# Performance work log

Measured on AMD Instinct MI355X. Metric: run time of the kernel, lower is better.

The kernel has to match this reference:

```python
import jax, jax.numpy as jnp
import numpy as np

NUM_HEADS = 16


def setup_inputs() -> dict:
    key = jax.random.key(0)
    ks = jax.random.split(key, 6)
    dim = 1024
    B, N = 4, 4096
    s = 1.0 / np.sqrt(dim)
    return {
        "x": jax.random.normal(ks[0], (B, N, dim), dtype=jnp.float32),
        "Wq": jax.random.normal(ks[1], (dim, dim), dtype=jnp.float32) * s,
        "Wk": jax.random.normal(ks[2], (dim, dim), dtype=jnp.float32) * s,
        "Wv": jax.random.normal(ks[3], (dim, dim), dtype=jnp.float32) * s,
        "Wo": jax.random.normal(ks[4], (dim, dim), dtype=jnp.float32) * s,
        "bo": jnp.zeros((dim,), dtype=jnp.float32),
    }


def reference(x, Wq, Wk, Wv, Wo, bo):
    # STAtten (linear attention) branch, no SNN, dropout = 0 (identity in eval).
    B, N, C = x.shape
    H = NUM_HEADS
    D = C // H
    scale = D ** (-0.5)

    def heads(W):
        # torch nn.Linear: y = x @ W.T ; then [B,N,H,D] -> [B,H,N,D]
        y = jnp.einsum('bnc,oc->bno', x, W)
        return y.reshape(B, N, H, D).transpose(0, 2, 1, 3)

    q = heads(Wq)
    k = heads(Wk)
    v = heads(Wv)

    kv = jnp.einsum('bhnd,bhne->bhde', k, v) * scale  # [B,H,D,D]
    out = jnp.einsum('bhnd,bhde->bhne', q, kv)        # [B,H,N,D]

    out = out.transpose(0, 2, 1, 3).reshape(B, N, C)
    return jnp.einsum('bnc,oc->bno', out, Wo) + bo
```

## Files before the change

kernel.cpp:

```cpp
#include <hip/hip_runtime.h>
#include <hip/hip_bf16.h>
#include <math.h>

typedef __hip_bfloat16 bf16;
typedef float f32x4 __attribute__((ext_vector_type(4)));
typedef short s16x8 __attribute__((ext_vector_type(8)));

typedef const __attribute__((address_space(1))) void* as1cvp;
typedef __attribute__((address_space(3))) void* as3vp;

__device__ __forceinline__ unsigned short f2bf(float f) {
  unsigned u = __float_as_uint(f);
  u += 0x7FFFu + ((u >> 16) & 1u);
  return (unsigned short)(u >> 16);
}
__device__ __forceinline__ float bf2f(unsigned short s) {
  return __uint_as_float(((unsigned)s) << 16);
}

__device__ __forceinline__ void gpu_barrier() {
  asm volatile("" ::: "memory");
  __builtin_amdgcn_s_barrier();
  asm volatile("" ::: "memory");
}

__device__ __forceinline__ void tri_decode(int xt, int* ti_out, int* tj_out) {
  int tj = (int)((sqrtf(8.0f * (float)xt + 1.0f) - 1.0f) * 0.5f);
  int tri = tj * (tj + 1) / 2;
  if (xt < tri) { --tj; tri = tj * (tj + 1) / 2; }
  else if (xt >= tri + tj + 1) { ++tj; tri = tj * (tj + 1) / 2; }
  *ti_out = xt - tri;
  *tj_out = tj;
}

__global__ __launch_bounds__(256) void cast_transpose(const float* __restrict__ x,
                                                      unsigned short* __restrict__ xb,
                                                      unsigned short* __restrict__ xT) {
  __shared__ unsigned short tl[128 * 136];
  const int n0 = blockIdx.x * 128, d0 = blockIdx.y * 128, b = blockIdx.z;
  const int t = threadIdx.x;

  const int rr0 = t >> 4;
  const int u   = t & 15;
  const int dd  = u * 8;
#pragma unroll
  for (int it = 0; it < 8; ++it) {
    const int rr = rr0 + it * 16;
    const float* src = x + ((long)(b * 4096 + n0 + rr)) * 1024 + d0 + dd;
    f32x4 v0 = *(const f32x4*)src;
    f32x4 v1 = *(const f32x4*)(src + 4);
    s16x8 o;
    o[0] = (short)f2bf(v0[0]); o[1] = (short)f2bf(v0[1]);
    o[2] = (short)f2bf(v0[2]); o[3] = (short)f2bf(v0[3]);
    o[4] = (short)f2bf(v1[0]); o[5] = (short)f2bf(v1[1]);
    o[6] = (short)f2bf(v1[2]); o[7] = (short)f2bf(v1[3]);
    *(s16x8*)&xb[((long)(b * 4096 + n0 + rr)) * 1024 + d0 + dd] = o;
    const int phys = u ^ (rr >> 3);
    *(s16x8*)&tl[rr * 136 + phys * 8] = o;
  }
  __syncthreads();

  const int nblk = t & 15, dblk = t >> 4;
  s16x8 row[8];
#pragma unroll
  for (int j = 0; j < 8; ++j) {
    const int n = nblk * 8 + j;
    const int phys = dblk ^ nblk;
    row[j] = *(const s16x8*)&tl[n * 136 + phys * 8];
  }
#pragma unroll
  for (int c = 0; c < 8; ++c) {
    s16x8 col;
#pragma unroll
    for (int j = 0; j < 8; ++j) col[j] = row[j][c];
    *(s16x8*)&xT[((long)(b * 1024 + d0 + dblk * 8 + c)) * 4096 + n0 + nblk * 8] = col;
  }
}

__global__ __launch_bounds__(256) void cast_weights(const float* __restrict__ Wq,
                                                    const float* __restrict__ Wk,
                                                    const float* __restrict__ Wv,
                                                    const float* __restrict__ Wo,
                                                    unsigned short* __restrict__ Wkb,
                                                    unsigned short* __restrict__ Wvb,
                                                    unsigned short* __restrict__ Wqb,
                                                    unsigned short* __restrict__ Wob) {
  const int i = blockIdx.x * 256 + threadIdx.x;
  const int seg = blockIdx.y;
  const long flat = (long)i * 8;
  const float* src = (seg == 0) ? Wk : (seg == 1) ? Wv : (seg == 2) ? Wq : Wo;
  f32x4 v0 = *(const f32x4*)&src[flat];
  f32x4 v1 = *(const f32x4*)&src[flat + 4];
  s16x8 o;
  o[0] = (short)f2bf(v0[0]); o[1] = (short)f2bf(v0[1]);
  o[2] = (short)f2bf(v0[2]); o[3] = (short)f2bf(v0[3]);
  o[4] = (short)f2bf(v1[0]); o[5] = (short)f2bf(v1[1]);
  o[6] = (short)f2bf(v1[2]); o[7] = (short)f2bf(v1[3]);
  unsigned short* dst = (seg == 0) ? Wkb : (seg == 1) ? Wvb : (seg == 2) ? Wqb : Wob;
  *(s16x8*)&dst[flat] = o;
}

template<bool OUTF32>
__global__ __launch_bounds__(512, 2) void gemm256(
    const bf16* __restrict__ A, int lda, long aOffY, long aOffZ,
    const bf16* __restrict__ Bt, int ldb, long btOffY, long btOffZ,
    void* __restrict__ Cv, int ldc, long cOffY, long cOffZ,
    const float* __restrict__ bias, int K, int NtN, int gridmode)
{
  __shared__ char lds[131072];

  const int Nx = gridDim.x, Ny = gridDim.y;
  const int lin = blockIdx.x + Nx * (blockIdx.y + Ny * blockIdx.z);
  const int tot = Nx * Ny * gridDim.z;
  const int swz = (lin & 7) * (tot >> 3) + (lin >> 3);
  const int xt = swz % Nx;
  const int r2 = swz / Nx;
  const int y = r2 % Ny, z = r2 / Ny;
  int ti, tj;
  if (gridmode == 1) {
    ti = (int)((0x3221110000ULL >> (4 * xt)) & 15);
    tj = (int)((0x3323213210ULL >> (4 * xt)) & 15);
  } else { ti = xt / NtN; tj = xt % NtN; }
  const int bm = ti * 256, bn = tj * 256;

  A  += (long)z * aOffZ + (long)y * aOffY;
  Bt += (long)z * btOffZ + (long)y * btOffY;

  const int tid  = threadIdx.x;
  const int wid  = tid >> 6;
  const int lane = tid & 63;
  const int wm = wid >> 2;
  const int wn = wid & 3;
  const int frow = lane & 15;
  const int fkb  = (lane >> 4) << 4;
  const unsigned xorv = (unsigned)((lane & 7) << 4);

  const int q0 = (tid * 16) ^ (((tid >> 3) & 7) << 4);
  const int q1 = (8192 + tid * 16) ^ (((tid >> 3) & 7) << 4);
  const int srow0 = q0 >> 7, scol0 = (q0 & 127) >> 1;
  const int srow1 = q1 >> 7, scol1 = (q1 & 127) >> 1;
  const bf16* ag0 = A  + (long)(bm + srow0) * lda + scol0;
  const bf16* ag1 = A  + (long)(bm + srow1) * lda + scol1;
  const bf16* bg0 = Bt + (long)(bn + srow0) * ldb + scol0;
  const bf16* bg1 = Bt + (long)(bn + srow1) * ldb + scol1;

#define STAGE_A(buf, half, kk) do {                                                  \
    __builtin_amdgcn_global_load_lds((as1cvp)(ag0 + (long)(half)*128*lda + (kk)),    \
        (as3vp)(lds + (buf)*32768 + (half)*16384 + wid*1024), 16, 0, 0);             \
    __builtin_amdgcn_global_load_lds((as1cvp)(ag1 + (long)(half)*128*lda + (kk)),    \
        (as3vp)(lds + (buf)*32768 + (half)*16384 + 8192 + wid*1024), 16, 0, 0);      \
  } while (0)
#define STAGE_B(buf, half, kk) do {                                                  \
    __builtin_amdgcn_global_load_lds((as1cvp)(bg0 + (long)(half)*128*ldb + (kk)),    \
        (as3vp)(lds + 65536 + (buf)*32768 + (half)*16384 + wid*1024), 16, 0, 0);     \
    __builtin_amdgcn_global_load_lds((as1cvp)(bg1 + (long)(half)*128*ldb + (kk)),    \
        (as3vp)(lds + 65536 + (buf)*32768 + (half)*16384 + 8192 + wid*1024), 16, 0, 0); \
  } while (0)

  const unsigned paBase = (unsigned)((wm * 64 + frow) * 128 + fkb);
  const unsigned pbBase = (unsigned)(((wn & 1) * 64 + frow) * 128 + fkb);
  const unsigned bHalf  = (unsigned)((wn >> 1) * 16384);

#define RD_A(dst, cur, Mh, mi, kh)                                                   \
  dst = *(const s16x8*)(lds + (cur)*32768 + (Mh)*16384 +                             \
                        ((paBase + (mi)*2048u + (kh)*64u) ^ xorv))
#define RD_B(dst, cur, nj, kh)                                                       \
  dst = *(const s16x8*)(lds + 65536 + (cur)*32768 + bHalf +                          \
                        ((pbBase + (nj)*2048u + (kh)*64u) ^ xorv))

#define MFMA16(base, bb)                                                             \
  __builtin_amdgcn_s_setprio(1);                                                     \
  _Pragma("unroll")                                                                  \
  for (int mi = 0; mi < 4; ++mi)                                                     \
    _Pragma("unroll")                                                                \
    for (int nj = 0; nj < 4; ++nj)                                                   \
      acc[(base) + mi][nj] = __builtin_amdgcn_mfma_f32_16x16x32_bf16(                \
          a[mi], bb[nj], acc[(base) + mi][nj], 0, 0, 0);                             \
  __builtin_amdgcn_s_setprio(0);

#define LGKM0 asm volatile("s_waitcnt lgkmcnt(0)" ::: "memory")
#define VM8   asm volatile("s_waitcnt vmcnt(8)" ::: "memory")

  f32x4 acc[8][4] = {};
  s16x8 a[4], b0[4], b1[4];
  const int NT = K >> 6;

  STAGE_A(0, 0, 0); STAGE_B(0, 0, 0); STAGE_B(0, 1, 0);
  STAGE_A(0, 1, 0);
  {
    const int kk = (NT > 1) ? 64 : 0;
    STAGE_A(1, 0, kk); STAGE_B(1, 0, kk); STAGE_B(1, 1, kk);
  }
  VM8;
  gpu_barrier();

  for (int t = 0; t < NT; ++t) {
    const int cur = t & 1, nxt = cur ^ 1;
    const int k1 = ((t + 1 < NT) ? (t + 1) : 0) * 64;
    const int k2 = ((t + 2 < NT) ? (t + 2) : 0) * 64;

#pragma unroll
    for (int mi = 0; mi < 4; ++mi) RD_A(a[mi], cur, 0, mi, 0);
#pragma unroll
    for (int nj = 0; nj < 4; ++nj) RD_B(b0[nj], cur, nj, 0);
    STAGE_A(nxt, 1, k1);
    gpu_barrier(); LGKM0;
    MFMA16(0, b0)
    gpu_barrier();

#pragma unroll
    for (int mi = 0; mi < 4; ++mi) RD_A(a[mi], cur, 0, mi, 1);
#pragma unroll
    for (int nj = 0; nj < 4; ++nj) RD_B(b1[nj], cur, nj, 1);
    gpu_barrier(); LGKM0;
    MFMA16(0, b1)
    VM8;
    gpu_barrier();

#pragma unroll
    for (int mi = 0; mi < 4; ++mi) RD_A(a[mi], cur, 1, mi, 0);
    STAGE_A(cur, 0, k2); STAGE_B(cur, 0, k2); STAGE_B(cur, 1, k2);
    gpu_barrier(); LGKM0;
    MFMA16(4, b0)
    gpu_barrier();

#pragma unroll
    for (int mi = 0; mi < 4; ++mi) RD_A(a[mi], cur, 1, mi, 1);
    gpu_barrier(); LGKM0;
    MFMA16(4, b1)
    VM8;
    gpu_barrier();
  }

  asm volatile("s_waitcnt vmcnt(0)" ::: "memory");

  const int crow0 = bm + wm * 64 + (lane >> 4) * 4;
  const int ccol0 = bn + wn * 64 + (lane & 15);
  if (OUTF32) {
    float* C = (float*)Cv + (long)z * cOffZ + (long)y * cOffY;
    float bs[4];
#pragma unroll
    for (int j = 0; j < 4; ++j) bs[j] = bias ? bias[ccol0 + j * 16] : 0.0f;
#pragma unroll
    for (int i = 0; i < 8; ++i) {
      const int row = crow0 + (i >> 2) * 128 + (i & 3) * 16;
#pragma unroll
      for (int j = 0; j < 4; ++j) {
        const int col = ccol0 + j * 16;
#pragma unroll
        for (int r = 0; r < 4; ++r)
          C[(long)(row + r) * ldc + col] = acc[i][j][r] + bs[j];
      }
    }
  } else {
    unsigned short* C = (unsigned short*)Cv + (long)z * cOffZ + (long)y * cOffY;
#pragma unroll
    for (int i = 0; i < 8; ++i) {
      const int row = crow0 + (i >> 2) * 128 + (i & 3) * 16;
#pragma unroll
      for (int j = 0; j < 4; ++j) {
        const int col = ccol0 + j * 16;
#pragma unroll
        for (int r = 0; r < 4; ++r)
          C[(long)(row + r) * ldc + col] = f2bf(acc[i][j][r]);
      }
    }
  }
#undef STAGE_A
#undef STAGE_B
#undef RD_A
#undef RD_B
#undef MFMA16
#undef LGKM0
#undef VM8
}

template<int MODE>
__global__ __launch_bounds__(256) void gemm128(
    const bf16* __restrict__ A0, const bf16* __restrict__ B0,
    void* __restrict__ Cv, const float* __restrict__ bias)
{
  __shared__ char lds[65536];

  const int Nx = gridDim.x;
  const int lin = blockIdx.x + Nx * blockIdx.y;
  const int tot = Nx * gridDim.y;
  const int swz = (lin & 7) * (tot >> 3) + (lin >> 3);
  const int xt = swz % Nx, yy = swz / Nx;

  const int lda = (MODE == 0) ? 4096 : 1024;
  const int ldb = lda;
  const int K   = 1024;
  int bm, bn;
  const bf16 *A, *Bt;
  if (MODE == 0) {
    int ti, tj; tri_decode(xt, &ti, &tj);
    bm = ti * 128; bn = tj * 128;
    const int z = yy >> 2, ys = yy & 3;
    A  = A0 + (long)z * 4194304 + ys * 1024;
    Bt = A;
  } else {
    bm = (xt >> 3) * 128; bn = (xt & 7) * 128;
    A  = A0;
    Bt = B0 + (long)yy * 1048576L;
  }

  const int tid  = threadIdx.x;
  const int wid  = tid >> 6;
  const int lane = tid & 63;
  const int wr = (wid >> 1) * 64, wc = (wid & 1) * 64;
  const int frow = lane & 15;
  const int fkb  = (lane >> 4) << 4;
  const unsigned xorv = (unsigned)((lane & 7) << 4);

  const int q0 = (tid * 16) ^ (((tid >> 3) & 7) << 4);
  const int srow0 = q0 >> 7, scol0 = (q0 & 127) >> 1;
  const bf16* ag = A  + (long)(bm + srow0) * lda + scol0;
  const bf16* bg = Bt + (long)(bn + srow0) * ldb + scol0;

#define STG128(buf, kk) do {                                                         \
    _Pragma("unroll")                                                                \
    for (int i = 0; i < 4; ++i) {                                                    \
      __builtin_amdgcn_global_load_lds((as1cvp)(ag + (long)i * 32 * lda + (kk)),     \
          (as3vp)(lds + (buf) * 16384 + i * 4096 + tid * 16), 16, 0, 0);             \
      __builtin_amdgcn_global_load_lds((as1cvp)(bg + (long)i * 32 * ldb + (kk)),     \
          (as3vp)(lds + 32768 + (buf) * 16384 + i * 4096 + tid * 16), 16, 0, 0);     \
    }                                                                                \
  } while (0)

  const unsigned paB = (unsigned)((wr + frow) * 128 + fkb);
  const unsigned pbB = (unsigned)((wc + frow) * 128 + fkb);

  f32x4 acc[4][4] = {};
  const int NT = K >> 6;

  STG128(0, 0);
  asm volatile("s_waitcnt vmcnt(0)" ::: "memory");
  gpu_barrier();

  for (int t = 0; t < NT; ++t) {
    const int cur = t & 1;
    if (t + 1 < NT) STG128(cur ^ 1, (t + 1) * 64);
    s16x8 a[4][2], b[4][2];
#pragma unroll
    for (int mi = 0; mi < 4; ++mi)
#pragma unroll
      for (int kh = 0; kh < 2; ++kh)
        a[mi][kh] = *(const s16x8*)(lds + cur * 16384 +
                                    ((paB + mi * 2048u + kh * 64u) ^ xorv));
#pragma unroll
    for (int nj = 0; nj < 4; ++nj)
#pragma unroll
      for (int kh = 0; kh < 2; ++kh)
        b[nj][kh] = *(const s16x8*)(lds + 32768 + cur * 16384 +
                                    ((pbB + nj * 2048u + kh * 64u) ^ xorv));
    asm volatile("s_waitcnt lgkmcnt(0)" ::: "memory");
#pragma unroll
    for (int mi = 0; mi < 4; ++mi)
#pragma unroll
      for (int nj = 0; nj < 4; ++nj) {
        acc[mi][nj] = __builtin_amdgcn_mfma_f32_16x16x32_bf16(a[mi][0], b[nj][0], acc[mi][nj], 0, 0, 0);
        acc[mi][nj] = __builtin_amdgcn_mfma_f32_16x16x32_bf16(a[mi][1], b[nj][1], acc[mi][nj], 0, 0, 0);
      }
    asm volatile("s_waitcnt vmcnt(0)" ::: "memory");
    gpu_barrier();
  }

  const int r0 = wr + (lane >> 4) * 4;
  const int c0t = wc + (lane & 15);
  if (MODE == 0) {
    unsigned short* C = (unsigned short*)Cv + (long)(yy * 36 + xt) * 16384;
#pragma unroll
    for (int mi = 0; mi < 4; ++mi)
#pragma unroll
      for (int nj = 0; nj < 4; ++nj)
#pragma unroll
        for (int r = 0; r < 4; ++r)
          C[(r0 + mi * 16 + r) * 128 + c0t + nj * 16] = f2bf(acc[mi][nj][r]);
  } else {
    unsigned short* C = (unsigned short*)Cv + (long)yy * 1048576;
#pragma unroll
    for (int mi = 0; mi < 4; ++mi)
#pragma unroll
      for (int nj = 0; nj < 4; ++nj)
#pragma unroll
        for (int r = 0; r < 4; ++r)
          C[(long)(bm + r0 + mi * 16 + r) * 1024 + bn + c0t + nj * 16] =
              f2bf(acc[mi][nj][r]);
  }
#undef STG128
}

__global__ __launch_bounds__(256) void gred128(const unsigned short* __restrict__ Gp,
                                               unsigned short* __restrict__ Gb) {
  const int tile = blockIdx.x >> 2, sub = blockIdx.x & 3;
  const int z = blockIdx.y;
  int ti, tj; tri_decode(tile, &ti, &tj);
  const int t = threadIdx.x;
  const int rr = sub * 32 + (t >> 3);
  const int c0 = (t & 7) * 16;

  float s[16] = {};
#pragma unroll
  for (int y = 0; y < 4; ++y) {
    const unsigned short* p = Gp + ((long)(z * 4 + y) * 36 + tile) * 16384 + rr * 128 + c0;
#pragma unroll
    for (int q = 0; q < 2; ++q) {
      s16x8 v = *(const s16x8*)&p[q * 8];
#pragma unroll
      for (int j = 0; j < 8; ++j) s[q * 8 + j] += bf2f((unsigned short)v[j]);
    }
  }
  unsigned short hi[16];
#pragma unroll
  for (int j = 0; j < 16; ++j) hi[j] = f2bf(s[j]);
  unsigned short* base = Gb + (long)z * 1048576;
  const int R0 = ti * 128 + rr, C0 = tj * 128 + c0;
#pragma unroll
  for (int q = 0; q < 2; ++q)
    *(s16x8*)&base[(long)R0 * 1024 + C0 + q * 8] = *(const s16x8*)&hi[q * 8];
  if (ti != tj) {
#pragma unroll
    for (int j = 0; j < 16; ++j)
      base[(long)(C0 + j) * 1024 + R0] = hi[j];
  }
}

template<int OUTMODE>
__global__ __launch_bounds__(256) void gemm64(
    const bf16* __restrict__ A, int lda, long aOffZ,
    const bf16* __restrict__ Bt, int ldb, long btOffZ,
    void* __restrict__ Cv, int ldc, long cOffZ, int loOff,
    int K, int NtN, int diag, int ksplit)
{
  __shared__ char lds[32768];

  const int Nx = gridDim.x;
  const int lin = blockIdx.x + Nx * blockIdx.y;
  const int tot = Nx * gridDim.y;
  const int swz = (lin & 7) * (tot >> 3) + (lin >> 3);
  const int xt = swz % Nx, y = swz / Nx;
  const int zb = y / ksplit, zs = y % ksplit;
  const int ti = diag ? xt : xt / NtN;
  const int tj = diag ? xt : xt % NtN;
  const int bm = ti * 64, bn = tj * 64;

  A  += (long)zb * aOffZ + (long)zs * K;
  Bt += (long)zb * btOffZ + (long)zs * K;

  const int tid  = threadIdx.x;
  const int wid  = tid >> 6;
  const int lane = tid & 63;
  const int wr = (wid >> 1) * 32, wc = (wid & 1) * 32;
  const int frow = lane & 15;
  const int fkb  = (lane >> 4) << 4;
  const unsigned xorv = (unsigned)((lane & 7) << 4);

  const int q0 = (tid * 16) ^ (((tid >> 3) & 7) << 4);
  const int q1 = (4096 + tid * 16) ^ (((tid >> 3) & 7) << 4);
  const int srow0 = q0 >> 7, scol0 = (q0 & 127) >> 1;
  const int srow1 = q1 >> 7, scol1 = (q1 & 127) >> 1;
  const bf16* ag0 = A  + (long)(bm + srow0) * lda + scol0;
  const bf16* ag1 = A  + (long)(bm + srow1) * lda + scol1;
  const bf16* bg0 = Bt + (long)(bn + srow0) * ldb + scol0;
  const bf16* bg1 = Bt + (long)(bn + srow1) * ldb + scol1;

#define STAGE64(buf, kk) do {                                                        \
    __builtin_amdgcn_global_load_lds((as1cvp)(ag0 + (kk)),                           \
        (as3vp)(lds + (buf)*8192 + wid*1024), 16, 0, 0);                             \
    __builtin_amdgcn_global_load_lds((as1cvp)(ag1 + (kk)),                           \
        (as3vp)(lds + (buf)*8192 + 4096 + wid*1024), 16, 0, 0);                      \
    __builtin_amdgcn_global_load_lds((as1cvp)(bg0 + (kk)),                           \
        (as3vp)(lds + 16384 + (buf)*8192 + wid*1024), 16, 0, 0);                     \
    __builtin_amdgcn_global_load_lds((as1cvp)(bg1 + (kk)),                           \
        (as3vp)(lds + 16384 + (buf)*8192 + 4096 + wid*1024), 16, 0, 0);              \
  } while (0)

  const unsigned paB = (unsigned)((wr + frow) * 128 + fkb);
  const unsigned pbB = (unsigned)((wc + frow) * 128 + fkb);

  f32x4 acc[2][2] = {};
  const int NT = K >> 6;

  STAGE64(0, 0);
  asm volatile("s_waitcnt vmcnt(0)" ::: "memory");
  gpu_barrier();

  for (int t = 0; t < NT; ++t) {
    const int cur = t & 1;
    if (t + 1 < NT) STAGE64(cur ^ 1, (t + 1) * 64);
    s16x8 a[2][2], b[2][2];
#pragma unroll
    for (int mi = 0; mi < 2; ++mi)
#pragma unroll
      for (int kh = 0; kh < 2; ++kh)
        a[mi][kh] = *(const s16x8*)(lds + cur * 8192 +
                                    ((paB + mi * 2048u + kh * 64u) ^ xorv));
#pragma unroll
    for (int nj = 0; nj < 2; ++nj)
#pragma unroll
      for (int kh = 0; kh < 2; ++kh)
        b[nj][kh] = *(const s16x8*)(lds + 16384 + cur * 8192 +
                                    ((pbB + nj * 2048u + kh * 64u) ^ xorv));
    asm volatile("s_waitcnt lgkmcnt(0)" ::: "memory");
#pragma unroll
    for (int mi = 0; mi < 2; ++mi)
#pragma unroll
      for (int nj = 0; nj < 2; ++nj) {
        acc[mi][nj] = __builtin_amdgcn_mfma_f32_16x16x32_bf16(a[mi][0], b[nj][0], acc[mi][nj], 0, 0, 0);
        acc[mi][nj] = __builtin_amdgcn_mfma_f32_16x16x32_bf16(a[mi][1], b[nj][1], acc[mi][nj], 0, 0, 0);
      }
    asm volatile("s_waitcnt vmcnt(0)" ::: "memory");
    gpu_barrier();
  }

  const int r0 = wr + (lane >> 4) * 4;
  const int c0 = wc + (lane & 15);
  if (OUTMODE == 1) {
    float* C = (float*)Cv + (long)y * cOffZ + (long)xt * 4096;
#pragma unroll
    for (int mi = 0; mi < 2; ++mi)
#pragma unroll
      for (int nj = 0; nj < 2; ++nj)
#pragma unroll
        for (int r = 0; r < 4; ++r)
          C[(r0 + mi * 16 + r) * 64 + c0 + nj * 16] = acc[mi][nj][r];
  } else {
    unsigned short* C = (unsigned short*)Cv + (long)y * cOffZ;
#pragma unroll
    for (int mi = 0; mi < 2; ++mi)
#pragma unroll
      for (int nj = 0; nj < 2; ++nj)
#pragma unroll
        for (int r = 0; r < 4; ++r) {
          const float v = acc[mi][nj][r];
          const unsigned short h = f2bf(v);
          const long idx = (long)(bm + r0 + mi * 16 + r) * ldc + bn + c0 + nj * 16;
          C[idx] = h;
          if (OUTMODE == 2) C[idx + loOff] = f2bf(v - bf2f(h));
        }
  }
#undef STAGE64
}

__global__ __launch_bounds__(256) void yt_kernel(const float* __restrict__ Up,
                                                 const unsigned short* __restrict__ Wqb,
                                                 unsigned short* __restrict__ Yt) {
  __shared__ float Ul[64 * 64];
  __shared__ float Wql[64 * 68];
  const int cblk = blockIdx.x, h = blockIdx.y, z = blockIdx.z;
  const int t = threadIdx.x;

  {
    const int d = t >> 2, e0 = (t & 3) * 16;
#pragma unroll
    for (int q = 0; q < 4; ++q) {
      f32x4 s = {};
#pragma unroll
      for (int sp = 0; sp < 4; ++sp) {
        f32x4 v = *(const f32x4*)&Up[((long)(z * 4 + sp) * 16 + h) * 4096 + d * 64 + e0 + q * 4];
#pragma unroll
        for (int j = 0; j < 4; ++j) s[j] += v[j];
      }
      *(f32x4*)&Ul[d * 64 + e0 + q * 4] = s;
    }
    const unsigned short* wp = Wqb + (long)(h * 64 + d) * 1024 + cblk * 64 + e0;
#pragma unroll
    for (int q = 0; q < 2; ++q) {
      s16x8 w = *(const s16x8*)&wp[q * 8];
#pragma unroll
      for (int j = 0; j < 8; ++j) Wql[d * 68 + e0 + q * 8 + j] = bf2f((unsigned short)w[j]);
    }
  }
  __syncthreads();

  const int jc = t >> 2, e0 = (t & 3) * 16;
  f32x4 acc[4] = {};
  for (int d = 0; d < 64; ++d) {
    const float w = Wql[d * 68 + jc];
    const float* ur = &Ul[d * 64 + e0];
#pragma unroll
    for (int q = 0; q < 4; ++q) {
      f32x4 u4 = *(const f32x4*)&ur[q * 4];
#pragma unroll
      for (int j = 0; j < 4; ++j) acc[q][j] += w * u4[j];
    }
  }
  unsigned short* yp = Yt + (long)z * 1048576 + (long)(cblk * 64 + jc) * 1024 + h * 64 + e0;
#pragma unroll
  for (int q = 0; q < 4; ++q)
#pragma unroll
    for (int j = 0; j < 4; ++j) yp[q * 4 + j] = f2bf(acc[q][j] * 0.125f);
}

extern "C" void kernel_launch(void* const* d_in, const int* in_sizes, int n_in,
                              void* d_out, int out_size, void* d_ws, size_t ws_size,
                              hipStream_t stream) {
  const float* x  = (const float*)d_in[0];
  const float* Wq = (const float*)d_in[1];
  const float* Wk = (const float*)d_in[2];
  const float* Wv = (const float*)d_in[3];
  const float* Wo = (const float*)d_in[4];
  const float* bo = (const float*)d_in[5];
  float* out = (float*)d_out;

  char* ws = (char*)d_ws;
  unsigned short* xb  = (unsigned short*)(ws);
  unsigned short* xT  = (unsigned short*)(ws + 33554432);
  unsigned short* Gb  = (unsigned short*)(ws + 33554432);
  unsigned short* Wkb = (unsigned short*)(ws + 67108864);
  unsigned short* Wvb = (unsigned short*)(ws + 71303168);
  unsigned short* Wqb = (unsigned short*)(ws + 75497472);
  unsigned short* Wob = (unsigned short*)(ws + 77594624);
  unsigned short* Gp  = (unsigned short*)(ws + 79691776);
  unsigned short* T   = (unsigned short*)(ws + 79691776);
  float*          Up  = (float*)         (ws + 96468992);
  unsigned short* Yt  = (unsigned short*)(ws + 113246208);
  unsigned short* R   = (unsigned short*)(ws + 121634816);

  cast_transpose<<<dim3(32, 8, 4), 256, 0, stream>>>(x, xb, xT);
  cast_weights<<<dim3(512, 4), 256, 0, stream>>>(Wq, Wk, Wv, Wo, Wkb, Wvb, Wqb, Wob);

  gemm128<0><<<dim3(36, 16), 256, 0, stream>>>(
      (const bf16*)xT, nullptr, (void*)Gp, nullptr);

  gred128<<<dim3(144, 4), 256, 0, stream>>>(Gp, Gb);

  gemm128<3><<<dim3(64, 4), 256, 0, stream>>>(
      (const bf16*)Wkb, (const bf16*)Gb, (void*)T, nullptr);

  gemm64<1><<<dim3(16, 16), 256, 0, stream>>>(
      (const bf16*)T, 1024, 1048576L, (const bf16*)Wvb, 1024, 0L,
      (void*)Up, 64, 65536L, 0, 256, 1, 1, 4);

  yt_kernel<<<dim3(16, 16, 4), 256, 0, stream>>>(Up, Wqb, Yt);

  gemm128<3><<<dim3(64, 4), 256, 0, stream>>>(
      (const bf16*)Wob, (const bf16*)Yt, (void*)R, nullptr);

  gemm256<true><<<dim3(64, 1, 4), 512, 0, stream>>>(
      (const bf16*)xb, 1024, 0L, 4194304L,
      (const bf16*)R, 1024, 0L, 1048576L,
      (void*)out, 1024, 0L, 4194304L,
      bo, 1024, 4, 0);
}
```

Baseline: 170.3 us.

## Replace split-K Gram GEMM plus reduction with single full-K 64-tile triangular GEMM

The Gram matrix xᵀx per batch was computed as a 128-tile triangular GEMM split four ways over K, writing bf16 partials that a separate reduction kernel summed and mirrored. It is now one 64-tile GEMM over the full K=4096, decoding upper-triangle tiles (136 per batch) and writing each tile plus its transpose directly. This removes the partial-sum traffic, an extra launch and the intermediate bf16 rounding. In exchange it uses smaller tiles with less reuse, only 544 blocks each running a long K loop, and uncoalesced transposed stores.

Result: faster. 166.5 us (-2.2%).

```diff
diff --git a/kernel.cpp b/kernel.cpp
--- a/kernel.cpp
+++ b/kernel.cpp
@@ -288,22 +288,12 @@
   const int swz = (lin & 7) * (tot >> 3) + (lin >> 3);
   const int xt = swz % Nx, yy = swz / Nx;
 
-  const int lda = (MODE == 0) ? 4096 : 1024;
-  const int ldb = lda;
+  const int lda = 1024;
+  const int ldb = 1024;
   const int K   = 1024;
-  int bm, bn;
-  const bf16 *A, *Bt;
-  if (MODE == 0) {
-    int ti, tj; tri_decode(xt, &ti, &tj);
-    bm = ti * 128; bn = tj * 128;
-    const int z = yy >> 2, ys = yy & 3;
-    A  = A0 + (long)z * 4194304 + ys * 1024;
-    Bt = A;
-  } else {
-    bm = (xt >> 3) * 128; bn = (xt & 7) * 128;
-    A  = A0;
-    Bt = B0 + (long)yy * 1048576L;
-  }
+  const int bm = (xt >> 3) * 128, bn = (xt & 7) * 128;
+  const bf16* A  = A0;
+  const bf16* Bt = B0 + (long)yy * 1048576L;
 
   const int tid  = threadIdx.x;
   const int wid  = tid >> 6;
@@ -368,62 +358,16 @@
 
   const int r0 = wr + (lane >> 4) * 4;
   const int c0t = wc + (lane & 15);
-  if (MODE == 0) {
-    unsigned short* C = (unsigned short*)Cv + (long)(yy * 36 + xt) * 16384;
-#pragma unroll
-    for (int mi = 0; mi < 4; ++mi)
-#pragma unroll
-      for (int nj = 0; nj < 4; ++nj)
-#pragma unroll
-        for (int r = 0; r < 4; ++r)
-          C[(r0 + mi * 16 + r) * 128 + c0t + nj * 16] = f2bf(acc[mi][nj][r]);
-  } else {
-    unsigned short* C = (unsigned short*)Cv + (long)yy * 1048576;
-#pragma unroll
-    for (int mi = 0; mi < 4; ++mi)
-#pragma unroll
-      for (int nj = 0; nj < 4; ++nj)
-#pragma unroll
-        for (int r = 0; r < 4; ++r)
-          C[(long)(bm + r0 + mi * 16 + r) * 1024 + bn + c0t + nj * 16] =
-              f2bf(acc[mi][nj][r]);
-  }
+  unsigned short* C = (unsigned short*)Cv + (long)yy * 1048576;
+#pragma unroll
+  for (int mi = 0; mi < 4; ++mi)
+#pragma unroll
+    for (int nj = 0; nj < 4; ++nj)
+#pragma unroll
+      for (int r = 0; r < 4; ++r)
+        C[(long)(bm + r0 + mi * 16 + r) * 1024 + bn + c0t + nj * 16] =
+            f2bf(acc[mi][nj][r]);
 #undef STG128
-}
-
-__global__ __launch_bounds__(256) void gred128(const unsigned short* __restrict__ Gp,
-                                               unsigned short* __restrict__ Gb) {
-  const int tile = blockIdx.x >> 2, sub = blockIdx.x & 3;
-  const int z = blockIdx.y;
-  int ti, tj; tri_decode(tile, &ti, &tj);
-  const int t = threadIdx.x;
-  const int rr = sub * 32 + (t >> 3);
-  const int c0 = (t & 7) * 16;
-
-  float s[16] = {};
-#pragma unroll
-  for (int y = 0; y < 4; ++y) {
-    const unsigned short* p = Gp + ((long)(z * 4 + y) * 36 + tile) * 16384 + rr * 128 + c0;
-#pragma unroll
-    for (int q = 0; q < 2; ++q) {
-      s16x8 v = *(const s16x8*)&p[q * 8];
-#pragma unroll
-      for (int j = 0; j < 8; ++j) s[q * 8 + j] += bf2f((unsigned short)v[j]);
-    }
-  }
-  unsigned short hi[16];
-#pragma unroll
-  for (int j = 0; j < 16; ++j) hi[j] = f2bf(s[j]);
-  unsigned short* base = Gb + (long)z * 1048576;
-  const int R0 = ti * 128 + rr, C0 = tj * 128 + c0;
-#pragma unroll
-  for (int q = 0; q < 2; ++q)
-    *(s16x8*)&base[(long)R0 * 1024 + C0 + q * 8] = *(const s16x8*)&hi[q * 8];
-  if (ti != tj) {
-#pragma unroll
-    for (int j = 0; j < 16; ++j)
-      base[(long)(C0 + j) * 1024 + R0] = hi[j];
-  }
 }
 
 template<int OUTMODE>
@@ -431,7 +375,7 @@
     const bf16* __restrict__ A, int lda, long aOffZ,
     const bf16* __restrict__ Bt, int ldb, long btOffZ,
     void* __restrict__ Cv, int ldc, long cOffZ, int loOff,
-    int K, int NtN, int diag, int ksplit)
+    int K, int NtN, int dmode, int ksplit)
 {
   __shared__ char lds[32768];
 
@@ -441,8 +385,10 @@
   const int swz = (lin & 7) * (tot >> 3) + (lin >> 3);
   const int xt = swz % Nx, y = swz / Nx;
   const int zb = y / ksplit, zs = y % ksplit;
-  const int ti = diag ? xt : xt / NtN;
-  const int tj = diag ? xt : xt % NtN;
+  int ti, tj;
+  if (dmode == 2)      { tri_decode(xt, &ti, &tj); }
+  else if (dmode == 1) { ti = xt; tj = xt; }
+  else                 { ti = xt / NtN; tj = xt % NtN; }
   const int bm = ti * 64, bn = tj * 64;
 
   A  += (long)zb * aOffZ + (long)zs * K;
@@ -525,6 +471,20 @@
 #pragma unroll
         for (int r = 0; r < 4; ++r)
           C[(r0 + mi * 16 + r) * 64 + c0 + nj * 16] = acc[mi][nj][r];
+  } else if (OUTMODE == 3) {
+    unsigned short* C = (unsigned short*)Cv + (long)y * cOffZ;
+#pragma unroll
+    for (int mi = 0; mi < 2; ++mi)
+#pragma unroll
+      for (int nj = 0; nj < 2; ++nj)
+#pragma unroll
+        for (int r = 0; r < 4; ++r) {
+          const unsigned short h = f2bf(acc[mi][nj][r]);
+          const int R = bm + r0 + mi * 16 + r;
+          const int Cc = bn + c0 + nj * 16;
+          C[(long)R * 1024 + Cc] = h;
+          if (ti != tj) C[(long)Cc * 1024 + R] = h;
+        }
   } else {
     unsigned short* C = (unsigned short*)Cv + (long)y * cOffZ;
 #pragma unroll
@@ -607,13 +567,12 @@
   char* ws = (char*)d_ws;
   unsigned short* xb  = (unsigned short*)(ws);
   unsigned short* xT  = (unsigned short*)(ws + 33554432);
-  unsigned short* Gb  = (unsigned short*)(ws + 33554432);
   unsigned short* Wkb = (unsigned short*)(ws + 67108864);
   unsigned short* Wvb = (unsigned short*)(ws + 71303168);
   unsigned short* Wqb = (unsigned short*)(ws + 75497472);
   unsigned short* Wob = (unsigned short*)(ws + 77594624);
-  unsigned short* Gp  = (unsigned short*)(ws + 79691776);
-  unsigned short* T   = (unsigned short*)(ws + 79691776);
+  unsigned short* Gb  = (unsigned short*)(ws + 79691776);
+  unsigned short* T   = (unsigned short*)(ws + 88080384);
   float*          Up  = (float*)         (ws + 96468992);
   unsigned short* Yt  = (unsigned short*)(ws + 113246208);
   unsigned short* R   = (unsigned short*)(ws + 121634816);
@@ -621,10 +580,9 @@
   cast_transpose<<<dim3(32, 8, 4), 256, 0, stream>>>(x, xb, xT);
   cast_weights<<<dim3(512, 4), 256, 0, stream>>>(Wq, Wk, Wv, Wo, Wkb, Wvb, Wqb, Wob);
 
-  gemm128<0><<<dim3(36, 16), 256, 0, stream>>>(
-      (const bf16*)xT, nullptr, (void*)Gp, nullptr);
-
-  gred128<<<dim3(144, 4), 256, 0, stream>>>(Gp, Gb);
+  gemm64<3><<<dim3(136, 4), 256, 0, stream>>>(
+      (const bf16*)xT, 4096, 4194304L, (const bf16*)xT, 4096, 4194304L,
+      (void*)Gb, 1024, 1048576L, 0, 4096, 1, 2, 1);
 
   gemm128<3><<<dim3(64, 4), 256, 0, stream>>>(
       (const bf16*)Wkb, (const bf16*)Gb, (void*)T, nullptr);
```
